# Performance work log

Measured on AMD Instinct MI355X. Metric: run time of the kernel, lower is better.

Reference implementation:

```python
import jax, jax.numpy as jnp
import numpy as np

N = 8192
F_IN = 1024
F_OUT = 512

def glorot(key, shape):
    limit = np.sqrt(6.0 / (shape[0] + shape[1]))
    return jax.random.uniform(key, shape, minval=-limit, maxval=limit, dtype=jnp.float32)

def setup_inputs() -> dict:
    key = jax.random.key(0)
    k1, k2, k3 = jax.random.split(key, 3)
    x = jax.random.normal(k1, (N, F_IN), dtype=jnp.float32)
    adj = jax.random.uniform(k2, (N, N), dtype=jnp.float32)  # dense nonnegative adjacency
    W = glorot(k3, (F_IN, F_OUT))
    b = jnp.zeros((F_OUT,), dtype=jnp.float32)
    return {"x": x, "adj": adj, "W": W, "b": b}

def reference(x, adj, W, b):
    # GCN layer: relu( D^{-1/2} (A + I) D^{-1/2} @ (x @ W) + b )
    n = adj.shape[0]
    A = adj + jnp.eye(n, dtype=adj.dtype)            # add self loops (tf.diag(In))
    d = jnp.sum(A, axis=1)                            # row-sum degrees
    d_is = d ** -0.5                                  # D^{-1/2}
    # D1 @ A @ D1 expressed as row/col scaling (identical math, no diag GEMMs)
    A_norm = A * d_is[:, None] * d_is[None, :]
    pre_sup = x @ W                                   # [N, F_OUT]
    out = A_norm @ pre_sup + b                        # propagation + bias
    return jax.nn.relu(out)
```

## Files before the change

kernel.cpp:

```cpp
#include <hip/hip_runtime.h>
#include <stdint.h>

#define NN 8192
#define FIN 1024
#define FOUT 512

typedef __attribute__((ext_vector_type(4))) float f32x4;
typedef __attribute__((ext_vector_type(8))) short s16x8;
typedef __attribute__((ext_vector_type(4))) unsigned short u16x4;

__device__ __forceinline__ short f2bf(float f) {
    return __builtin_bit_cast(short, static_cast<__bf16>(f));
}
__device__ __forceinline__ float bf2f(short s) {
    return (float)__builtin_bit_cast(__bf16, s);
}

__global__ __launch_bounds__(256) void rowsum_cvt_kernel(const float* __restrict__ adj,
                                                         short* __restrict__ adjB,
                                                         float* __restrict__ d_is) {
    const int row = blockIdx.x;
    const float4* a = reinterpret_cast<const float4*>(adj + (size_t)row * NN);
    u16x4* ob = reinterpret_cast<u16x4*>(adjB + (size_t)row * NN);
    float s = 0.f;
    #pragma unroll 2
    for (int j = threadIdx.x; j < NN / 4; j += 256) {
        float4 v = a[j];
        s += (v.x + v.y) + (v.z + v.w);
        u16x4 p;
        p[0] = (unsigned short)f2bf(v.x); p[1] = (unsigned short)f2bf(v.y);
        p[2] = (unsigned short)f2bf(v.z); p[3] = (unsigned short)f2bf(v.w);
        ob[j] = p;
    }
    #pragma unroll
    for (int off = 32; off > 0; off >>= 1) s += __shfl_down(s, off, 64);
    __shared__ float red[4];
    if ((threadIdx.x & 63) == 0) red[threadIdx.x >> 6] = s;
    __syncthreads();
    if (threadIdx.x == 0) {
        const float d = red[0] + red[1] + red[2] + red[3] + 1.0f;
        d_is[row] = 1.0f / sqrtf(d);
    }
}

__global__ __launch_bounds__(256) void rowsum_kernel(const float* __restrict__ adj,
                                                     float* __restrict__ d_is) {
    const int row = blockIdx.x;
    const float4* a = reinterpret_cast<const float4*>(adj + (size_t)row * NN);
    float s = 0.f;
    #pragma unroll 4
    for (int j = threadIdx.x; j < NN / 4; j += 256) {
        float4 v = a[j];
        s += (v.x + v.y) + (v.z + v.w);
    }
    #pragma unroll
    for (int off = 32; off > 0; off >>= 1) s += __shfl_down(s, off, 64);
    __shared__ float red[4];
    if ((threadIdx.x & 63) == 0) red[threadIdx.x >> 6] = s;
    __syncthreads();
    if (threadIdx.x == 0) {
        const float d = red[0] + red[1] + red[2] + red[3] + 1.0f;
        d_is[row] = 1.0f / sqrtf(d);
    }
}

__global__ __launch_bounds__(256) void cvt_x_kernel(const float* __restrict__ x,
                                                    short* __restrict__ xB) {
    const size_t i = ((size_t)blockIdx.x * 256 + threadIdx.x) * 8;
    const float4 v0 = *reinterpret_cast<const float4*>(&x[i]);
    const float4 v1 = *reinterpret_cast<const float4*>(&x[i + 4]);
    s16x8 o;
    o[0] = f2bf(v0.x); o[1] = f2bf(v0.y); o[2] = f2bf(v0.z); o[3] = f2bf(v0.w);
    o[4] = f2bf(v1.x); o[5] = f2bf(v1.y); o[6] = f2bf(v1.z); o[7] = f2bf(v1.w);
    *reinterpret_cast<s16x8*>(&xB[i]) = o;
}

__global__ __launch_bounds__(256) void wt_kernel(const float* __restrict__ W,
                                                 short* __restrict__ WT) {
    __shared__ float T[64][68];
    const int wc = blockIdx.x;
    const int wk = blockIdx.y;
    const int t = threadIdx.x;
    const int cc = (t & 15) * 4;
    #pragma unroll
    for (int i = 0; i < 4; ++i) {
        const int rr = (t >> 4) + i * 16;
        *reinterpret_cast<float4*>(&T[rr][cc]) =
            *reinterpret_cast<const float4*>(&W[(size_t)(wk * 64 + rr) * FOUT + wc * 64 + cc]);
    }
    __syncthreads();
    const int a = t >> 2;
    const int b0 = (t & 3) * 16;
    s16x8 v0, v1;
    #pragma unroll
    for (int e = 0; e < 8; ++e) { v0[e] = f2bf(T[b0 + e][a]); v1[e] = f2bf(T[b0 + 8 + e][a]); }
    short* dst = &WT[(size_t)(wc * 64 + a) * FIN + wk * 64 + b0];
    *reinterpret_cast<s16x8*>(dst) = v0;
    *reinterpret_cast<s16x8*>(dst + 8) = v1;
}

__global__ __launch_bounds__(256, 4) void xwg_kernel(const short* __restrict__ xB,
                                                     const short* __restrict__ WT,
                                                     const float* __restrict__ d_is,
                                                     short* __restrict__ psT) {
    constexpr int NT = FIN / 32;
    __shared__ short As[2][4096];
    __shared__ short Bs[2][2048];

    const int tid = threadIdx.x;
    const int lin = blockIdx.x;
    const int swz = (lin & 7) * 64 + (lin >> 3);
    const int col0 = (swz & 7) * 64;
    const int row0 = (swz >> 3) * 128;

    const int lane = tid & 63;
    const int wv = tid >> 6;
    const int wr = wv >> 1, wc = wv & 1;
    const int l15 = lane & 15;
    const int kq = lane >> 4;
    const int xorv = (l15 & 12) << 2;

    int arow[2], acoff[2];
    #pragma unroll
    for (int i = 0; i < 2; ++i) {
        const int slot = i * 256 + tid;
        const int P = (slot << 4) ^ (slot & 48);
        arow[i] = P >> 6;
        acoff[i] = (P & 63) >> 1;
    }
    const short* Ab = xB + (size_t)row0 * FIN;
    const short* Bb = WT + (size_t)col0 * FIN;

    auto stage = [&](int buf, int k0) {
        #pragma unroll
        for (int i = 0; i < 2; ++i) {
            const short* src = Ab + (size_t)arow[i] * FIN + k0 + acoff[i];
            short* dst = &As[buf][(i * 256 + (tid & 192)) * 8];
            __builtin_amdgcn_global_load_lds(
                (const __attribute__((address_space(1))) unsigned int*)src,
                (__attribute__((address_space(3))) unsigned int*)dst, 16, 0, 0);
        }
        {
            const short* src = Bb + (size_t)arow[0] * FIN + k0 + acoff[0];
            short* dst = &Bs[buf][(tid & 192) * 8];
            __builtin_amdgcn_global_load_lds(
                (const __attribute__((address_space(1))) unsigned int*)src,
                (__attribute__((address_space(3))) unsigned int*)dst, 16, 0, 0);
        }
    };

    f32x4 acc[4][2] = {};
    auto compute = [&](int buf) {
        s16x8 af[4], bfr[2];
        #pragma unroll
        for (int m = 0; m < 4; ++m) {
            const int byteoff = ((wr * 64 + m * 16 + l15) * 64 + kq * 16) ^ xorv;
            af[m] = *reinterpret_cast<const s16x8*>(&As[buf][byteoff >> 1]);
        }
        #pragma unroll
        for (int n = 0; n < 2; ++n) {
            const int byteoff = ((wc * 32 + n * 16 + l15) * 64 + kq * 16) ^ xorv;
            bfr[n] = *reinterpret_cast<const s16x8*>(&Bs[buf][byteoff >> 1]);
        }
        #pragma unroll
        for (int m = 0; m < 4; ++m)
            #pragma unroll
            for (int n = 0; n < 2; ++n)
                acc[m][n] = __builtin_amdgcn_mfma_f32_16x16x32_bf16(af[m], bfr[n], acc[m][n], 0, 0, 0);
    };

    stage(0, 0);
    __syncthreads();
    int cur = 0;
    for (int t = 0; t < NT; ++t) {
        if (t + 1 < NT) stage(cur ^ 1, (t + 1) * 32);
        compute(cur);
        __syncthreads();
        cur ^= 1;
    }

    #pragma unroll
    for (int m = 0; m < 4; ++m) {
        const int rbase = row0 + wr * 64 + m * 16 + kq * 4;
        float dr[4];
        #pragma unroll
        for (int j = 0; j < 4; ++j) dr[j] = d_is[rbase + j];
        #pragma unroll
        for (int n = 0; n < 2; ++n) {
            const int col = col0 + wc * 32 + n * 16 + l15;
            u16x4 pk;
            #pragma unroll
            for (int j = 0; j < 4; ++j) pk[j] = (unsigned short)f2bf(dr[j] * acc[m][n][j]);
            *reinterpret_cast<u16x4*>(&psT[(size_t)col * NN + rbase]) = pk;
        }
    }
}

__global__ __launch_bounds__(256, 4) void prop2_kernel(
    const short* __restrict__ adjB, const short* __restrict__ psT,
    short* __restrict__ Pb0, short* __restrict__ Pb1,
    short* __restrict__ Pb2, float* __restrict__ Pf) {
    constexpr int Ksub = NN / 4;
    constexpr int NT = Ksub / 32;
    __shared__ short As[2][4096];
    __shared__ short Bs[2][4096];

    const int tid = threadIdx.x;
    const int lin = blockIdx.x;
    const int swz = (lin & 7) * 128 + (lin >> 3);
    const int col0 = (swz & 3) * 128;
    const int ks = (swz >> 2) & 3;
    const int row0 = (swz >> 4) * 128;

    const int lane = tid & 63;
    const int wv = tid >> 6;
    const int wr = wv >> 1, wc = wv & 1;
    const int l15 = lane & 15;
    const int kq = lane >> 4;
    const int xorv = (l15 & 12) << 2;

    int arow[2], acoff[2];
    #pragma unroll
    for (int i = 0; i < 2; ++i) {
        const int slot = i * 256 + tid;
        const int P = (slot << 4) ^ (slot & 48);
        arow[i] = P >> 6;
        acoff[i] = (P & 63) >> 1;
    }
    const size_t kbase = (size_t)ks * Ksub;
    const short* Ab = adjB + (size_t)row0 * NN + kbase;
    const short* Bb = psT + (size_t)col0 * NN + kbase;

    auto stage = [&](int buf, int k0) {
        #pragma unroll
        for (int i = 0; i < 2; ++i) {
            const short* src = Ab + (size_t)arow[i] * NN + k0 + acoff[i];
            short* dst = &As[buf][(i * 256 + (tid & 192)) * 8];
            __builtin_amdgcn_global_load_lds(
                (const __attribute__((address_space(1))) unsigned int*)src,
                (__attribute__((address_space(3))) unsigned int*)dst, 16, 0, 0);
        }
        #pragma unroll
        for (int i = 0; i < 2; ++i) {
            const short* src = Bb + (size_t)arow[i] * NN + k0 + acoff[i];
            short* dst = &Bs[buf][(i * 256 + (tid & 192)) * 8];
            __builtin_amdgcn_global_load_lds(
                (const __attribute__((address_space(1))) unsigned int*)src,
                (__attribute__((address_space(3))) unsigned int*)dst, 16, 0, 0);
        }
    };

    f32x4 acc[4][4] = {};
    auto compute = [&](int buf) {
        s16x8 af[4], bfr[4];
        #pragma unroll
        for (int m = 0; m < 4; ++m) {
            const int byteoff = ((wr * 64 + m * 16 + l15) * 64 + kq * 16) ^ xorv;
            af[m] = *reinterpret_cast<const s16x8*>(&As[buf][byteoff >> 1]);
        }
        #pragma unroll
        for (int n = 0; n < 4; ++n) {
            const int byteoff = ((wc * 64 + n * 16 + l15) * 64 + kq * 16) ^ xorv;
            bfr[n] = *reinterpret_cast<const s16x8*>(&Bs[buf][byteoff >> 1]);
        }
        #pragma unroll
        for (int m = 0; m < 4; ++m)
            #pragma unroll
            for (int n = 0; n < 4; ++n)
                acc[m][n] = __builtin_amdgcn_mfma_f32_16x16x32_bf16(af[m], bfr[n], acc[m][n], 0, 0, 0);
    };

    stage(0, 0);
    __syncthreads();
    int cur = 0;
    for (int t = 0; t < NT; ++t) {
        if (t + 1 < NT) stage(cur ^ 1, (t + 1) * 32);
        compute(cur);
        __syncthreads();
        cur ^= 1;
    }

    if (ks == 3) {
        #pragma unroll
        for (int m = 0; m < 4; ++m) {
            const int rbase = row0 + wr * 64 + m * 16 + kq * 4;
            #pragma unroll
            for (int n = 0; n < 4; ++n) {
                const int col = col0 + wc * 64 + n * 16 + l15;
                #pragma unroll
                for (int j = 0; j < 4; ++j)
                    Pf[(size_t)(rbase + j) * FOUT + col] = acc[m][n][j];
            }
        }
    } else {
        short* Pt = (ks == 0) ? Pb0 : (ks == 1) ? Pb1 : Pb2;
        #pragma unroll
        for (int m = 0; m < 4; ++m) {
            const int rbase = row0 + wr * 64 + m * 16 + kq * 4;
            #pragma unroll
            for (int n = 0; n < 4; ++n) {
                const int col = col0 + wc * 64 + n * 16 + l15;
                #pragma unroll
                for (int j = 0; j < 4; ++j)
                    Pt[(size_t)(rbase + j) * FOUT + col] = f2bf(acc[m][n][j]);
            }
        }
    }
}

__global__ __launch_bounds__(256) void ep4_kernel(
    const short* __restrict__ Pb0, const short* __restrict__ Pb1,
    const short* __restrict__ Pb2, float* __restrict__ out,
    const short* __restrict__ psT, const float* __restrict__ d_is,
    const float* __restrict__ bias) {
    const int col0 = blockIdx.x * 128;
    const int row0 = blockIdx.y * 32;
    const int t = threadIdx.x;
    const int c = col0 + (t & 31) * 4;
    const float4 bb = *reinterpret_cast<const float4*>(&bias[c]);
    #pragma unroll
    for (int it = 0; it < 4; ++it) {
        const int r = row0 + (t >> 5) + it * 8;
        const size_t idx = (size_t)r * FOUT + c;
        const u16x4 a = *reinterpret_cast<const u16x4*>(&Pb0[idx]);
        const u16x4 b4 = *reinterpret_cast<const u16x4*>(&Pb1[idx]);
        const u16x4 c4 = *reinterpret_cast<const u16x4*>(&Pb2[idx]);
        const float4 d4 = *reinterpret_cast<const float4*>(&out[idx]);
        const float dr = d_is[r];
        float s[4], o4[4];
        #pragma unroll
        for (int j = 0; j < 4; ++j) s[j] = bf2f(psT[(size_t)(c + j) * NN + r]);
        const float dd[4] = {d4.x, d4.y, d4.z, d4.w};
        const float bbv[4] = {bb.x, bb.y, bb.z, bb.w};
        #pragma unroll
        for (int j = 0; j < 4; ++j) {
            const float sum = ((bf2f((short)a[j]) + bf2f((short)b4[j])) +
                               (bf2f((short)c4[j]) + dd[j])) + s[j];
            o4[j] = fmaxf(dr * sum + bbv[j], 0.f);
        }
        float4 o = {o4[0], o4[1], o4[2], o4[3]};
        *reinterpret_cast<float4*>(&out[idx]) = o;
    }
}

template<int KLEN, int MODE>
__global__ __launch_bounds__(256, 4) void gemm_kernel(
    const float* __restrict__ A, const short* __restrict__ B,
    const float* __restrict__ d_is,
    short* __restrict__ psT,
    float* __restrict__ P0, float* __restrict__ P1) {
    constexpr int KS = (MODE == 1) ? 2 : 1;
    constexpr int Ksub = KLEN / KS;
    constexpr int NT = Ksub / 32;
    constexpr int LDA = 40;
    __shared__ short As[2][128 * LDA];
    __shared__ short Bs[2][64 * LDA];

    const int tid = threadIdx.x;
    const int nchunk = gridDim.x >> 3;
    const int lin = blockIdx.x;
    const int swz = (lin & 7) * nchunk + (lin >> 3);
    const int col0 = (swz & 7) * 64;
    const int yp = (swz >> 3) & 63;
    const int ks = swz >> 9;
    const int row0 = yp * 128;
    const int kbase = ks * Ksub;

    const int lane = tid & 63;
    const int wv = tid >> 6;
    const int wr = wv >> 1, wc = wv & 1;
    const int l15 = lane & 15;
    const int koff = (lane >> 4) * 8;

    const int ar = tid >> 1, ak = (tid & 1) * 16;
    const float* Abase = A + (size_t)(row0 + ar) * KLEN + kbase + ak;
    const int br = tid >> 2, bk = (tid & 3) * 8;
    const short* Bbase = B + (size_t)(col0 + br) * KLEN + kbase + bk;

    float4 qa0, qa1, qa2, qa3;
    s16x8 qb;
    auto loadG = [&](int k0) {
        const float4* p = reinterpret_cast<const float4*>(Abase + k0);
        qa0 = p[0]; qa1 = p[1]; qa2 = p[2]; qa3 = p[3];
        qb = *reinterpret_cast<const s16x8*>(Bbase + k0);
    };
    auto writeL = [&](int buf) {
        const float a[16] = {qa0.x, qa0.y, qa0.z, qa0.w, qa1.x, qa1.y, qa1.z, qa1.w,
                             qa2.x, qa2.y, qa2.z, qa2.w, qa3.x, qa3.y, qa3.z, qa3.w};
        s16x8 v0, v1;
        #pragma unroll
        for (int e = 0; e < 8; ++e) { v0[e] = f2bf(a[e]); v1[e] = f2bf(a[8 + e]); }
        *reinterpret_cast<s16x8*>(&As[buf][ar * LDA + ak]) = v0;
        *reinterpret_cast<s16x8*>(&As[buf][ar * LDA + ak + 8]) = v1;
        *reinterpret_cast<s16x8*>(&Bs[buf][br * LDA + bk]) = qb;
    };

    f32x4 acc[4][2] = {};
    auto compute = [&](int buf) {
        s16x8 af[4], bfr[2];
        #pragma unroll
        for (int m = 0; m < 4; ++m)
            af[m] = *reinterpret_cast<const s16x8*>(&As[buf][(wr * 64 + m * 16 + l15) * LDA + koff]);
        #pragma unroll
        for (int n = 0; n < 2; ++n)
            bfr[n] = *reinterpret_cast<const s16x8*>(&Bs[buf][(wc * 32 + n * 16 + l15) * LDA + koff]);
        #pragma unroll
        for (int m = 0; m < 4; ++m)
            #pragma unroll
            for (int n = 0; n < 2; ++n)
                acc[m][n] = __builtin_amdgcn_mfma_f32_16x16x32_bf16(af[m], bfr[n], acc[m][n], 0, 0, 0);
    };

    loadG(0);
    writeL(0);
    __syncthreads();
    int cur = 0;
    for (int t = 0; t < NT; ++t) {
        if (t + 1 < NT) loadG((t + 1) * 32);
        compute(cur);
        if (t + 1 < NT) writeL(cur ^ 1);
        __syncthreads();
        cur ^= 1;
    }

    if (MODE == 0) {
        #pragma unroll
        for (int m = 0; m < 4; ++m) {
            const int rbase = row0 + wr * 64 + m * 16 + (lane >> 4) * 4;
            float dr[4];
            #pragma unroll
            for (int j = 0; j < 4; ++j) dr[j] = d_is[rbase + j];
            #pragma unroll
            for (int n = 0; n < 2; ++n) {
                const int col = col0 + wc * 32 + n * 16 + l15;
                u16x4 pk;
                #pragma unroll
                for (int j = 0; j < 4; ++j) pk[j] = (unsigned short)f2bf(dr[j] * acc[m][n][j]);
                *reinterpret_cast<u16x4*>(&psT[(size_t)col * NN + rbase]) = pk;
            }
        }
    } else {
        float* tgt = (ks == 0) ? P0 : P1;
        #pragma unroll
        for (int m = 0; m < 4; ++m) {
            const int rbase = row0 + wr * 64 + m * 16 + (lane >> 4) * 4;
            #pragma unroll
            for (int n = 0; n < 2; ++n) {
                const int col = col0 + wc * 32 + n * 16 + l15;
                f32x4 v = acc[m][n];
                if (ks == 0) {
                    const u16x4 sv = *reinterpret_cast<const u16x4*>(&psT[(size_t)col * NN + rbase]);
                    #pragma unroll
                    for (int j = 0; j < 4; ++j) v[j] += bf2f((short)sv[j]);
                }
                #pragma unroll
                for (int j = 0; j < 4; ++j)
                    tgt[(size_t)(rbase + j) * FOUT + col] = v[j];
            }
        }
    }
}

__global__ __launch_bounds__(256) void ep_kernel(const float* __restrict__ P0,
                                                 float* __restrict__ out,
                                                 const float* __restrict__ d_is,
                                                 const float* __restrict__ bias) {
    const size_t idx = ((size_t)blockIdx.x * 256 + threadIdx.x) * 4;
    const int row = (int)(idx >> 9);
    const int col = (int)(idx & 511);
    const float4 p0 = *reinterpret_cast<const float4*>(&P0[idx]);
    const float4 p1 = *reinterpret_cast<const float4*>(&out[idx]);
    const float4 bb = *reinterpret_cast<const float4*>(&bias[col]);
    const float dr = d_is[row];
    float4 o;
    o.x = fmaxf(dr * (p0.x + p1.x) + bb.x, 0.f);
    o.y = fmaxf(dr * (p0.y + p1.y) + bb.y, 0.f);
    o.z = fmaxf(dr * (p0.z + p1.z) + bb.z, 0.f);
    o.w = fmaxf(dr * (p0.w + p1.w) + bb.w, 0.f);
    *reinterpret_cast<float4*>(&out[idx]) = o;
}

extern "C" void kernel_launch(void* const* d_in, const int* in_sizes, int n_in,
                              void* d_out, int out_size, void* d_ws, size_t ws_size,
                              hipStream_t stream) {
    const float* x   = (const float*)d_in[0];
    const float* adj = (const float*)d_in[1];
    const float* W   = (const float*)d_in[2];
    const float* b   = (const float*)d_in[3];
    float* out = (float*)d_out;

    const size_t NEED = (size_t)FOUT * NN * 2 + (size_t)FOUT * FIN * 2
                      + (size_t)NN * FIN * 2 + 3ull * NN * FOUT * 2
                      + NN * 4 + (size_t)NN * NN * 2;

    if (ws_size >= NEED) {
        short* psT = (short*)d_ws;
        short* WT  = psT + (size_t)FOUT * NN;
        short* xB  = WT + (size_t)FOUT * FIN;
        short* Pb0 = xB + (size_t)NN * FIN;
        short* Pb1 = Pb0 + (size_t)NN * FOUT;
        short* Pb2 = Pb1 + (size_t)NN * FOUT;
        float* dis = (float*)(Pb2 + (size_t)NN * FOUT);
        short* adjB = (short*)(dis + NN);

        hipLaunchKernelGGL(rowsum_cvt_kernel, dim3(NN), dim3(256), 0, stream, adj, adjB, dis);
        hipLaunchKernelGGL(cvt_x_kernel, dim3(NN * FIN / 2048), dim3(256), 0, stream, x, xB);
        hipLaunchKernelGGL(wt_kernel, dim3(8, 16), dim3(256), 0, stream, W, WT);
        hipLaunchKernelGGL(xwg_kernel, dim3(512), dim3(256), 0, stream, xB, WT, dis, psT);
        hipLaunchKernelGGL(prop2_kernel, dim3(1024), dim3(256), 0, stream,
                           adjB, psT, Pb0, Pb1, Pb2, out);
        hipLaunchKernelGGL(ep4_kernel, dim3(4, 256), dim3(256), 0, stream,
                           Pb0, Pb1, Pb2, out, psT, dis, b);
    } else {
        short* psT = (short*)d_ws;
        short* WT  = psT + (size_t)FOUT * NN;
        float* P0  = (float*)(WT + (size_t)FOUT * FIN);
        float* dis = P0 + (size_t)NN * FOUT;

        hipLaunchKernelGGL(rowsum_kernel, dim3(NN), dim3(256), 0, stream, adj, dis);
        hipLaunchKernelGGL(wt_kernel, dim3(8, 16), dim3(256), 0, stream, W, WT);
        hipLaunchKernelGGL((gemm_kernel<FIN, 0>), dim3(512), dim3(256), 0, stream,
                           x, WT, dis, psT, nullptr, nullptr);
        hipLaunchKernelGGL((gemm_kernel<NN, 1>), dim3(1024), dim3(256), 0, stream,
                           adj, psT, dis, psT, P0, out);
        hipLaunchKernelGGL(ep_kernel, dim3(NN * FOUT / 1024), dim3(256), 0, stream,
                           P0, out, dis, b);
    }
}
```

Measured before the change: 225.3 us.

## Prefetch two tiles ahead with manual vmcnt waits in both GEMM loops

Both bf16 MFMA GEMM main loops now issue loads for tiles t and t+1 up front and, each iteration, wait with s_waitcnt vmcnt(N) only for the older tile's loads before a raw s_barrier. The buffer just consumed is then refilled with tile t+2. This replaces the __syncthreads-based single-tile lookahead, keeping more global loads in flight and avoiding full memory drains at each barrier. It depends on the stage() functions issuing exactly the counted number of vector memory ops (likely direct-to-LDS loads). It also relies on hand-written waitcnt values being correct, which is fragile.

```diff
diff --git a/kernel.cpp b/kernel.cpp
--- a/kernel.cpp
+++ b/kernel.cpp
@@ -170,12 +170,21 @@
     };
 
     stage(0, 0);
-    __syncthreads();
+    stage(1, 32);
     int cur = 0;
+    #pragma unroll 1
     for (int t = 0; t < NT; ++t) {
-        if (t + 1 < NT) stage(cur ^ 1, (t + 1) * 32);
+        if (t < NT - 1) {
+            asm volatile("s_waitcnt vmcnt(3)" ::: "memory");
+        } else {
+            asm volatile("s_waitcnt vmcnt(0)" ::: "memory");
+        }
+        __builtin_amdgcn_s_barrier();
         compute(cur);
-        __syncthreads();
+        if (t + 2 < NT) {
+            __builtin_amdgcn_s_barrier();
+            stage(cur, (t + 2) * 32);
+        }
         cur ^= 1;
     }
 
@@ -271,12 +280,21 @@
     };
 
     stage(0, 0);
-    __syncthreads();
+    stage(1, 32);
     int cur = 0;
+    #pragma unroll 1
     for (int t = 0; t < NT; ++t) {
-        if (t + 1 < NT) stage(cur ^ 1, (t + 1) * 32);
+        if (t < NT - 1) {
+            asm volatile("s_waitcnt vmcnt(4)" ::: "memory");
+        } else {
+            asm volatile("s_waitcnt vmcnt(0)" ::: "memory");
+        }
+        __builtin_amdgcn_s_barrier();
         compute(cur);
-        __syncthreads();
+        if (t + 2 < NT) {
+            __builtin_amdgcn_s_barrier();
+            stage(cur, (t + 2) * 32);
+        }
         cur ^= 1;
     }
 
```

After: 218.1 us. 1.03x faster.
